# Kernel optimization log

Hardware: AMD Instinct MI355X
Metric: run time of the kernel (lower is better)

Reference implementation:

```python
import jax, jax.numpy as jnp
import numpy as np

N = 50000      # nodes
E = 800000     # edges in adj1/adj2 (avg degree 16)
ED = 400000    # edges after edge-drop
IN = 256       # input feature dim
H = 128        # hidden
H2 = 256       # 2*hidden
GATE = 64


def _xavier(key, shape):
    fan_in, fan_out = shape[0], shape[1]
    lim = np.sqrt(6.0 / (fan_in + fan_out)).astype(np.float32)
    return jax.random.uniform(key, shape, jnp.float32, -lim, lim)


def setup_inputs() -> dict:
    key = jax.random.key(0)
    ks = jax.random.split(key, 20)
    d = {}
    d["x1"] = jax.random.normal(ks[0], (N, IN), jnp.float32)
    d["x2"] = jax.random.normal(ks[1], (N, IN), jnp.float32)
    d["adj1_row"] = jax.random.randint(ks[2], (E,), 0, N, jnp.int32)
    d["adj1_col"] = jax.random.randint(ks[3], (E,), 0, N, jnp.int32)
    d["adj1_val"] = jax.random.uniform(ks[4], (E,), jnp.float32)
    d["adj2_row"] = jax.random.randint(ks[5], (E,), 0, N, jnp.int32)
    d["adj2_col"] = jax.random.randint(ks[6], (E,), 0, N, jnp.int32)
    d["adj2_val"] = jax.random.uniform(ks[7], (E,), jnp.float32)
    d["drop_row"] = jax.random.randint(ks[8], (ED,), 0, N, jnp.int32)
    d["drop_col"] = jax.random.randint(ks[9], (ED,), 0, N, jnp.int32)
    d["drop_val"] = jax.random.uniform(ks[10], (ED,), jnp.float32)
    d["deg"] = jax.random.uniform(ks[11], (N, 1), jnp.float32)
    # GCN layer 0: Linear(IN -> 2H) no bias in fc, plus GCN bias + PReLU
    d["W0"] = _xavier(ks[12], (IN, H2))
    d["b0"] = jnp.zeros((H2,), jnp.float32)
    d["a0"] = jnp.full((1,), 0.25, jnp.float32)  # PReLU param
    # GCN layer 1: Linear(2H -> H)
    d["W1"] = _xavier(ks[13], (H2, H))
    d["b1"] = jnp.zeros((H,), jnp.float32)
    d["a1"] = jnp.full((1,), 0.25, jnp.float32)
    # MLP gate
    d["G1w"] = _xavier(ks[14], (H, GATE))
    d["G1b"] = jnp.zeros((GATE,), jnp.float32)
    d["G2w"] = _xavier(ks[15], (H, GATE))
    d["G2b"] = jnp.zeros((GATE,), jnp.float32)
    d["G3w"] = _xavier(ks[16], (2 * GATE + 1, 1))
    d["G3b"] = jnp.zeros((1,), jnp.float32)
    return d


def _spmm(row, col, val, x, n):
    # sparse adj @ x : gather source features, scale by edge value, scatter-add to rows
    return jax.ops.segment_sum(val[:, None] * x[col], row, num_segments=n)


def _prelu(x, a):
    return jnp.where(x >= 0, x, a * x)


def reference(x1, x2, adj1_row, adj1_col, adj1_val, adj2_row, adj2_col, adj2_val,
              drop_row, drop_col, drop_val, deg,
              W0, b0, a0, W1, b1, a1, G1w, G1b, G2w, G2b, G3w, G3b):
    n = x1.shape[0]

    def gcn(x, row, col, val, W, b, a):
        return _prelu(_spmm(row, col, val, x @ W, n) + b, a)

    def branch(x, row, col, val):
        h = jax.nn.relu(gcn(x, row, col, val, W0, b0, a0))
        return gcn(h, row, col, val, W1, b1, a1)

    # dropout on x1/x2 is identity in eval mode
    h1 = branch(x1, adj1_row, adj1_col, adj1_val)
    h2 = branch(x2, adj1_row, adj1_col, adj1_val)
    h3 = branch(x1, adj2_row, adj2_col, adj2_val)
    h4 = branch(x1, drop_row, drop_col, drop_val)

    # MLP gate on detached h1, h3, deg
    z1 = jax.lax.stop_gradient(h1) @ G1w + G1b
    z2 = jax.lax.stop_gradient(h3) @ G2w + G2b
    w = jnp.concatenate([z1, z2, jax.lax.stop_gradient(deg)], axis=1)
    beta = jax.nn.sigmoid(w @ G3w + G3b)
    return (h1, h2, h3, h4, beta)
```

## Files before the change

### kernel.cpp

```cpp
#include <hip/hip_runtime.h>
#include <hip/hip_bf16.h>

#define H2C 256
#define HDC 128
#define GATEC 64
#define FBSH 9
#define NBF 320
#define EPB 8192
#define EPBH 2048
#define CAPB 10240

typedef unsigned short ushort_t;
typedef unsigned long long ull_t;
typedef __attribute__((ext_vector_type(8))) __bf16 bf16x8;
typedef __attribute__((ext_vector_type(4))) float f32x4;

__device__ inline float bf2f(unsigned short v) {
    union { unsigned u; float f; } t; t.u = ((unsigned)v) << 16; return t.f;
}
__device__ inline unsigned short f2bf(float v) {
    __hip_bfloat16 b = __float2bfloat16(v);
    return *reinterpret_cast<unsigned short*>(&b);
}

__device__ inline void gload_lds16(const void* g, void* l) {
    __builtin_amdgcn_global_load_lds(
        (const __attribute__((address_space(1))) unsigned int*)g,
        (__attribute__((address_space(3))) unsigned int*)l, 16, 0, 0);
}

__global__ __launch_bounds__(256)
void gemm_bf16_mfma(const ushort_t* __restrict__ A, const ushort_t* __restrict__ BT,
                    ushort_t* __restrict__ C, int M, int Nn, int K)
{
    __shared__ ushort_t Alds[128 * 64];
    __shared__ ushort_t Blds[128 * 64];
    const int tid  = threadIdx.x;
    const int w    = tid >> 6;
    const int lane = tid & 63;
    const int wr   = w >> 1;
    const int wc   = w & 1;
    const int bm   = blockIdx.y * 128;
    const int bn   = blockIdx.x * 128;

    f32x4 acc[4][4] = {};

    for (int k0 = 0; k0 < K; k0 += 64) {
        #pragma unroll
        for (int i = 0; i < 4; ++i) {
            const int lin = i * 256 + tid;
            const int r = lin >> 3, p = lin & 7;
            int rm = bm + r; if (rm >= M) rm = M - 1;
            const ushort_t* ga = A + (size_t)rm * K + k0 + ((p ^ (r & 7)) << 3);
            gload_lds16(ga, &Alds[i * 2048 + w * 512]);
        }
        #pragma unroll
        for (int i = 0; i < 4; ++i) {
            const int lin = i * 256 + tid;
            const int r = lin >> 3, p = lin & 7;
            const ushort_t* gb = BT + (size_t)(bn + r) * K + k0 + ((p ^ (r & 7)) << 3);
            gload_lds16(gb, &Blds[i * 2048 + w * 512]);
        }
        __syncthreads();
        #pragma unroll
        for (int kk = 0; kk < 2; ++kk) {
            bf16x8 af[4], bfr[4];
            #pragma unroll
            for (int m = 0; m < 4; ++m) {
                const int r = wr * 64 + m * 16 + (lane & 15);
                const int s = kk * 4 + (lane >> 4);
                af[m] = *reinterpret_cast<const bf16x8*>(&Alds[r * 64 + ((s ^ (r & 7)) << 3)]);
            }
            #pragma unroll
            for (int n = 0; n < 4; ++n) {
                const int r = wc * 64 + n * 16 + (lane & 15);
                const int s = kk * 4 + (lane >> 4);
                bfr[n] = *reinterpret_cast<const bf16x8*>(&Blds[r * 64 + ((s ^ (r & 7)) << 3)]);
            }
            #pragma unroll
            for (int m = 0; m < 4; ++m)
                #pragma unroll
                for (int n = 0; n < 4; ++n)
                    acc[m][n] = __builtin_amdgcn_mfma_f32_16x16x32_bf16(
                        af[m], bfr[n], acc[m][n], 0, 0, 0);
        }
        __syncthreads();
    }

    #pragma unroll
    for (int m = 0; m < 4; ++m) {
        const int row0 = bm + wr * 64 + m * 16 + ((lane >> 4) << 2);
        #pragma unroll
        for (int n = 0; n < 4; ++n) {
            const int col = bn + wc * 64 + n * 16 + (lane & 15);
            #pragma unroll
            for (int q = 0; q < 4; ++q) {
                const int row = row0 + q;
                if (row < M) C[(size_t)row * Nn + col] = f2bf(acc[m][n][q]);
            }
        }
    }
}

__global__ __launch_bounds__(256)
void gemm_xw_f32(const float* __restrict__ X1, const float* __restrict__ X2,
                 const ushort_t* __restrict__ BT, ushort_t* __restrict__ C,
                 int M, int Nn, int K, int Mh)
{
    __shared__ float    Af[128 * 64];
    __shared__ ushort_t Blds[128 * 64];
    const int tid  = threadIdx.x;
    const int w    = tid >> 6;
    const int lane = tid & 63;
    const int wr   = w >> 1;
    const int wc   = w & 1;
    const int bm   = blockIdx.y * 128;
    const int bn   = blockIdx.x * 128;

    f32x4 acc[4][4] = {};

    for (int k0 = 0; k0 < K; k0 += 64) {
        #pragma unroll
        for (int i = 0; i < 8; ++i) {
            const int lin = i * 256 + tid;
            const int r = lin >> 4, q = lin & 15;
            int rm = bm + r; if (rm >= M) rm = M - 1;
            const float* src = ((rm < Mh) ? X1 + (size_t)rm * K
                                          : X2 + (size_t)(rm - Mh) * K)
                               + k0 + ((q ^ (r & 15)) << 2);
            gload_lds16(src, &Af[i * 1024 + w * 256]);
        }
        #pragma unroll
        for (int i = 0; i < 4; ++i) {
            const int lin = i * 256 + tid;
            const int r = lin >> 3, p = lin & 7;
            const ushort_t* gb = BT + (size_t)(bn + r) * K + k0 + ((p ^ (r & 7)) << 3);
            gload_lds16(gb, &Blds[i * 2048 + w * 512]);
        }
        __syncthreads();
        #pragma unroll
        for (int kk = 0; kk < 2; ++kk) {
            bf16x8 af[4], bfr[4];
            #pragma unroll
            for (int m = 0; m < 4; ++m) {
                const int r = wr * 64 + m * 16 + (lane & 15);
                const int s = kk * 4 + (lane >> 4);
                const int rx = r & 15;
                const float4 fa = *reinterpret_cast<const float4*>(
                    &Af[r * 64 + (((2 * s) ^ rx) << 2)]);
                const float4 fb = *reinterpret_cast<const float4*>(
                    &Af[r * 64 + (((2 * s + 1) ^ rx) << 2)]);
                ushort_t t[8] = {f2bf(fa.x), f2bf(fa.y), f2bf(fa.z), f2bf(fa.w),
                                 f2bf(fb.x), f2bf(fb.y), f2bf(fb.z), f2bf(fb.w)};
                af[m] = *reinterpret_cast<bf16x8*>(t);
            }
            #pragma unroll
            for (int n = 0; n < 4; ++n) {
                const int r = wc * 64 + n * 16 + (lane & 15);
                const int s = kk * 4 + (lane >> 4);
                bfr[n] = *reinterpret_cast<const bf16x8*>(&Blds[r * 64 + ((s ^ (r & 7)) << 3)]);
            }
            #pragma unroll
            for (int m = 0; m < 4; ++m)
                #pragma unroll
                for (int n = 0; n < 4; ++n)
                    acc[m][n] = __builtin_amdgcn_mfma_f32_16x16x32_bf16(
                        af[m], bfr[n], acc[m][n], 0, 0, 0);
        }
        __syncthreads();
    }

    #pragma unroll
    for (int m = 0; m < 4; ++m) {
        const int row0 = bm + wr * 64 + m * 16 + ((lane >> 4) << 2);
        #pragma unroll
        for (int n = 0; n < 4; ++n) {
            const int col = bn + wc * 64 + n * 16 + (lane & 15);
            #pragma unroll
            for (int q = 0; q < 4; ++q) {
                const int row = row0 + q;
                if (row < M) C[(size_t)row * Nn + col] = f2bf(acc[m][n][q]);
            }
        }
    }
}

__global__ __launch_bounds__(256)
void transpose2_f2bf_kernel(const float* __restrict__ W0, const float* __restrict__ W1,
                            ushort_t* __restrict__ W0T, ushort_t* __restrict__ W1T)
{
    int i = blockIdx.x * blockDim.x + threadIdx.x;
    if (i < H2C * H2C) {
        const int c = i / H2C, r = i % H2C;
        W0T[(size_t)c * H2C + r] = f2bf(W0[(size_t)r * H2C + c]);
    } else {
        i -= H2C * H2C;
        if (i < H2C * HDC) {
            const int c = i / H2C, r = i % H2C;
            W1T[(size_t)c * H2C + r] = f2bf(W1[(size_t)r * HDC + c]);
        }
    }
}

__global__ __launch_bounds__(256)
void bucket_hist_kernel(const int* __restrict__ r0, const int* __restrict__ r1_,
                        const int* __restrict__ rD, int E, int ED, int N,
                        int* __restrict__ bcnt)
{
    __shared__ int h[NBF];
    const int tid = threadIdx.x;
    for (int t = tid; t < NBF; t += 256) h[t] = 0;
    __syncthreads();
    const long long tot = 2LL * E + ED;
    const long long base = (long long)blockIdx.x * EPBH;
    #pragma unroll
    for (int k = 0; k < EPBH / 256; ++k) {
        const long long i = base + k * 256 + tid;
        if (i < tot) {
            int vr;
            if (i < E)            vr = r0[i];
            else if (i < 2LL * E) vr = N + r1_[i - E];
            else                  vr = 2 * N + rD[i - 2LL * E];
            atomicAdd(&h[vr >> FBSH], 1);
        }
    }
    __syncthreads();
    for (int t = tid; t < NBF; t += 256)
        if (h[t]) atomicAdd(&bcnt[t], h[t]);
}

__global__ void scan_buckets_kernel(const int* __restrict__ bcnt, int nbu, int tot,
                                    int* __restrict__ boff, int* __restrict__ gcur,
                                    int* __restrict__ g, int NR)
{
    if (threadIdx.x == 0) {
        int acc = 0;
        for (int t = 0; t < nbu; ++t) { boff[t] = acc; gcur[t] = acc; acc += bcnt[t]; }
        boff[nbu] = acc;
        g[NR] = tot;
    }
}

__global__ __launch_bounds__(256)
void bucket_stage_kernel(const int* __restrict__ r0, const int* __restrict__ c0, const float* __restrict__ v0,
                         const int* __restrict__ r1, const int* __restrict__ c1, const float* __restrict__ v1,
                         const int* __restrict__ rD, const int* __restrict__ cD, const float* __restrict__ vD,
                         int E, int ED, int N,
                         int* __restrict__ gcur, ull_t* __restrict__ stg)
{
    __shared__ int hcnt[NBF];
    __shared__ int hbase[NBF];
    const int tid = threadIdx.x;
    for (int t = tid; t < NBF; t += 256) hcnt[t] = 0;
    __syncthreads();
    const long long tot = 2LL * E + ED;
    const long long base = (long long)blockIdx.x * EPB;
    #pragma unroll
    for (int k = 0; k < EPB / 256; ++k) {
        const long long i = base + k * 256 + tid;
        if (i < tot) {
            int vr;
            if (i < E)            vr = r0[i];
            else if (i < 2LL * E) vr = N + r1[i - E];
            else                  vr = 2 * N + rD[i - 2LL * E];
            atomicAdd(&hcnt[vr >> FBSH], 1);
        }
    }
    __syncthreads();
    for (int t = tid; t < NBF; t += 256) {
        const int c = hcnt[t];
        hbase[t] = c ? atomicAdd(&gcur[t], c) : 0;
        hcnt[t] = 0;
    }
    __syncthreads();
    #pragma unroll
    for (int k = 0; k < EPB / 256; ++k) {
        const long long i = base + k * 256 + tid;
        if (i < tot) {
            int vr, cc; float vv;
            if (i < E)            { vr = r0[i];                 cc = c0[i];            vv = v0[i]; }
            else if (i < 2LL * E) { vr = N + r1[i - E];         cc = c1[i - E];        vv = v1[i - E]; }
            else                  { vr = 2 * N + rD[i - 2LL * E]; cc = cD[i - 2LL * E]; vv = vD[i - 2LL * E]; }
            const int fb = vr >> FBSH;
            const int p = hbase[fb] + atomicAdd(&hcnt[fb], 1);
            stg[p] = ((ull_t)(unsigned)vr << 32) | ((unsigned)cc << 16) | f2bf(vv);
        }
    }
}

__global__ __launch_bounds__(256)
void sort_bucket_kernel(const int* __restrict__ boff, int NR,
                        const ull_t* __restrict__ stg,
                        int* __restrict__ g, unsigned* __restrict__ ecv)
{
    __shared__ int hcnt[512];
    __shared__ int hscan[512];
    __shared__ unsigned pay[CAPB];
    const int b = blockIdx.x;
    const int r0 = b << FBSH;
    if (r0 >= NR) return;
    int r1 = r0 + (1 << FBSH); if (r1 > NR) r1 = NR;
    const int nrows = r1 - r0;
    const int base = boff[b], end = boff[b + 1];
    const int bsz = end - base;
    const int tid = threadIdx.x;
    hcnt[tid] = 0; hcnt[tid + 256] = 0;
    __syncthreads();
    for (int i = base + tid; i < end; i += 256)
        atomicAdd(&hcnt[(int)(stg[i] >> 32) - r0], 1);
    __syncthreads();
    hscan[tid] = hcnt[tid]; hscan[tid + 256] = hcnt[tid + 256];
    __syncthreads();
    for (int o = 1; o < 512; o <<= 1) {
        const int a0 = (tid >= o) ? hscan[tid - o] : 0;
        const int a1 = (tid + 256 >= o) ? hscan[tid + 256 - o] : 0;
        __syncthreads();
        hscan[tid] += a0; hscan[tid + 256] += a1;
        __syncthreads();
    }
    if (tid < nrows)       g[r0 + tid]       = base + hscan[tid] - hcnt[tid];
    if (tid + 256 < nrows) g[r0 + tid + 256] = base + hscan[tid + 256] - hcnt[tid + 256];
    hcnt[tid]       = hscan[tid] - hcnt[tid];
    hcnt[tid + 256] = hscan[tid + 256] - hcnt[tid + 256];
    __syncthreads();
    if (bsz <= CAPB) {
        for (int i = base + tid; i < end; i += 256) {
            const ull_t t = stg[i];
            const int p = atomicAdd(&hcnt[(int)(t >> 32) - r0], 1);
            pay[p] = (unsigned)t;
        }
        __syncthreads();
        for (int i = tid; i < bsz; i += 256)
            ecv[base + i] = pay[i];
    } else {
        for (int i = base + tid; i < end; i += 256) {
            const ull_t t = stg[i];
            const int p = atomicAdd(&hcnt[(int)(t >> 32) - r0], 1);
            ecv[base + p] = (unsigned)t;
        }
    }
}

__global__ __launch_bounds__(256)
void spmm_f256(const int* __restrict__ rp, const unsigned* __restrict__ ecv,
               const ushort_t* __restrict__ X, ushort_t* __restrict__ Y,
               const float* __restrict__ bias, const float* __restrict__ ap, int n)
{
    const int r = blockIdx.x * 4 + (threadIdx.x >> 6);
    if (r >= n) return;
    const int lane = threadIdx.x & 63;
    const int half = lane >> 5;
    const int l    = lane & 31;
    const int s = rp[r], e = rp[r + 1];
    float acc[8] = {};
    #pragma unroll 4
    for (int j = s + half; j < e; j += 2) {
        const unsigned ev = ecv[j];
        const float v = bf2f((ushort_t)ev);
        const uint4 x = *reinterpret_cast<const uint4*>(X + (size_t)(ev >> 16) * H2C + l * 8);
        acc[0] += v * bf2f((ushort_t)x.x); acc[1] += v * bf2f((ushort_t)(x.x >> 16));
        acc[2] += v * bf2f((ushort_t)x.y); acc[3] += v * bf2f((ushort_t)(x.y >> 16));
        acc[4] += v * bf2f((ushort_t)x.z); acc[5] += v * bf2f((ushort_t)(x.z >> 16));
        acc[6] += v * bf2f((ushort_t)x.w); acc[7] += v * bf2f((ushort_t)(x.w >> 16));
    }
    #pragma unroll
    for (int k = 0; k < 8; ++k) acc[k] += __shfl_xor(acc[k], 32);
    if (half == 0) {
        const float a = ap[0];
        const int f0 = l * 8;
        const float4 b0v = *reinterpret_cast<const float4*>(bias + f0);
        const float4 b1v = *reinterpret_cast<const float4*>(bias + f0 + 4);
        const float bb[8] = {b0v.x, b0v.y, b0v.z, b0v.w, b1v.x, b1v.y, b1v.z, b1v.w};
        unsigned o[4];
        #pragma unroll
        for (int k = 0; k < 8; k += 2) {
            float tx = acc[k] + bb[k];
            float ty = acc[k + 1] + bb[k + 1];
            tx = tx >= 0.f ? tx : a * tx;  ty = ty >= 0.f ? ty : a * ty;
            tx = fmaxf(tx, 0.f);           ty = fmaxf(ty, 0.f);
            o[k >> 1] = ((unsigned)f2bf(ty) << 16) | f2bf(tx);
        }
        *reinterpret_cast<uint4*>(Y + (size_t)r * H2C + f0) = make_uint4(o[0], o[1], o[2], o[3]);
    }
}

__global__ __launch_bounds__(256)
void spmm_f128(const int* __restrict__ rp, const unsigned* __restrict__ ecv,
               const ushort_t* __restrict__ X, float* __restrict__ Y,
               const float* __restrict__ bias, const float* __restrict__ ap, int n)
{
    const int r = blockIdx.x * 4 + (threadIdx.x >> 6);
    if (r >= n) return;
    const int lane = threadIdx.x & 63;
    const int q = lane >> 4;
    const int l = lane & 15;
    const int s = rp[r], e = rp[r + 1];
    float acc[8] = {};
    #pragma unroll 4
    for (int j = s + q; j < e; j += 4) {
        const unsigned ev = ecv[j];
        const float v = bf2f((ushort_t)ev);
        const uint4 x = *reinterpret_cast<const uint4*>(X + (size_t)(ev >> 16) * HDC + l * 8);
        acc[0] += v * bf2f((ushort_t)x.x); acc[1] += v * bf2f((ushort_t)(x.x >> 16));
        acc[2] += v * bf2f((ushort_t)x.y); acc[3] += v * bf2f((ushort_t)(x.y >> 16));
        acc[4] += v * bf2f((ushort_t)x.z); acc[5] += v * bf2f((ushort_t)(x.z >> 16));
        acc[6] += v * bf2f((ushort_t)x.w); acc[7] += v * bf2f((ushort_t)(x.w >> 16));
    }
    #pragma unroll
    for (int k = 0; k < 8; ++k) {
        acc[k] += __shfl_xor(acc[k], 16);
        acc[k] += __shfl_xor(acc[k], 32);
    }
    if (q == 0) {
        const float a = ap[0];
        const int f0 = l * 8;
        const float4 b0v = *reinterpret_cast<const float4*>(bias + f0);
        const float4 b1v = *reinterpret_cast<const float4*>(bias + f0 + 4);
        const float bb[8] = {b0v.x, b0v.y, b0v.z, b0v.w, b1v.x, b1v.y, b1v.z, b1v.w};
        float o[8];
        #pragma unroll
        for (int k = 0; k < 8; ++k) {
            float t = acc[k] + bb[k];
            o[k] = t >= 0.f ? t : a * t;
        }
        *reinterpret_cast<float4*>(Y + (size_t)r * HDC + f0)     = make_float4(o[0], o[1], o[2], o[3]);
        *reinterpret_cast<float4*>(Y + (size_t)r * HDC + f0 + 4) = make_float4(o[4], o[5], o[6], o[7]);
    }
}

__global__ void gate_pre_kernel(const float* __restrict__ G1w, const float* __restrict__ G1b,
                                const float* __restrict__ G2w, const float* __restrict__ G2b,
                                const float* __restrict__ G3w, const float* __restrict__ G3b,
                                float* __restrict__ U)
{
    const int h = threadIdx.x;
    float s1 = 0.f, s2 = 0.f;
    for (int g = 0; g < GATEC; ++g) {
        s1 += G1w[h * GATEC + g] * G3w[g];
        s2 += G2w[h * GATEC + g] * G3w[GATEC + g];
    }
    U[h] = s1;
    U[HDC + h] = s2;
    if (h == 0) {
        float c = G3b[0];
        for (int g = 0; g < GATEC; ++g)
            c += G1b[g] * G3w[g] + G2b[g] * G3w[GATEC + g];
        U[2 * HDC] = c;
        U[2 * HDC + 1] = G3w[2 * GATEC];
    }
}

__global__ __launch_bounds__(256)
void beta_kernel(const float* __restrict__ h1, const float* __restrict__ h3,
                 const float* __restrict__ deg, const float* __restrict__ U,
                 float* __restrict__ beta, int n)
{
    const int i = blockIdx.x * blockDim.x + threadIdx.x;
    if (i >= n) return;
    const float c = U[2 * HDC], wd = U[2 * HDC + 1];
    float s = c + wd * deg[i];
    const float4* h1p = reinterpret_cast<const float4*>(h1 + (size_t)i * HDC);
    const float4* h3p = reinterpret_cast<const float4*>(h3 + (size_t)i * HDC);
    const float4* u1p = reinterpret_cast<const float4*>(U);
    const float4* u2p = reinterpret_cast<const float4*>(U + HDC);
    #pragma unroll 8
    for (int j = 0; j < HDC / 4; ++j) {
        const float4 a = h1p[j], b = u1p[j];
        s += a.x * b.x + a.y * b.y + a.z * b.z + a.w * b.w;
        const float4 a2 = h3p[j], b2 = u2p[j];
        s += a2.x * b2.x + a2.y * b2.y + a2.z * b2.z + a2.w * b2.w;
    }
    beta[i] = 1.f / (1.f + expf(-s));
}

extern "C" void kernel_launch(void* const* d_in, const int* in_sizes, int n_in,
                              void* d_out, int out_size, void* d_ws, size_t ws_size,
                              hipStream_t stream)
{
    const float* x1  = (const float*)d_in[0];
    const float* x2  = (const float*)d_in[1];
    const int*   a1r = (const int*)d_in[2];
    const int*   a1c = (const int*)d_in[3];
    const float* a1v = (const float*)d_in[4];
    const int*   a2r = (const int*)d_in[5];
    const int*   a2c = (const int*)d_in[6];
    const float* a2v = (const float*)d_in[7];
    const int*   dr  = (const int*)d_in[8];
    const int*   dc  = (const int*)d_in[9];
    const float* dv  = (const float*)d_in[10];
    const float* deg = (const float*)d_in[11];
    const float* W0  = (const float*)d_in[12];
    const float* b0  = (const float*)d_in[13];
    const float* a0  = (const float*)d_in[14];
    const float* W1  = (const float*)d_in[15];
    const float* b1  = (const float*)d_in[16];
    const float* a1p = (const float*)d_in[17];
    const float* G1w = (const float*)d_in[18];
    const float* G1b = (const float*)d_in[19];
    const float* G2w = (const float*)d_in[20];
    const float* G2b = (const float*)d_in[21];
    const float* G3w = (const float*)d_in[22];
    const float* G3b = (const float*)d_in[23];

    const int E  = in_sizes[2];
    const int ED = in_sizes[8];
    const int N  = in_sizes[11];
    const int IN = in_sizes[0] / N;
    const long long TOT = 2LL * E + ED;
    const int NR  = 3 * N;
    const int NBUSED = (NR + (1 << FBSH) - 1) >> FBSH;

    char* base = (char*)d_ws;
    size_t off = 0;
    auto alloc = [&](size_t bytes) -> char* {
        char* p = base + off;
        off += (bytes + 255) & ~(size_t)255;
        return p;
    };
    ushort_t* XW12b = (ushort_t*)alloc((size_t)2 * N * H2C * 2);
    char* R = alloc((size_t)N * H2C * 2 + (size_t)N * HDC * 2);
    ull_t*    stg  = (ull_t*)R;
    ushort_t* Bbb  = (ushort_t*)R;
    ushort_t* Cbb  = (ushort_t*)(R + (size_t)N * H2C * 2);
    ushort_t* W0T  = (ushort_t*)alloc((size_t)H2C * H2C * 2);
    ushort_t* W1T  = (ushort_t*)alloc((size_t)HDC * H2C * 2);
    float*    U    = (float*)alloc(258 * 4);
    int*  g       = (int*)alloc((size_t)(NR + 1) * 4);
    int*  bcnt    = (int*)alloc(NBF * 4);
    int*  boff    = (int*)alloc((NBF + 1) * 4);
    int*  gcur    = (int*)alloc(NBF * 4);
    unsigned* ecv = (unsigned*)alloc((size_t)TOT * 4);

    float* out  = (float*)d_out;
    float* h1   = out;
    float* h2   = out + 1 * (size_t)N * HDC;
    float* h3   = out + 2 * (size_t)N * HDC;
    float* h4   = out + 3 * (size_t)N * HDC;
    float* beta = out + 4 * (size_t)N * HDC;

    gate_pre_kernel<<<1, HDC, 0, stream>>>(G1w, G1b, G2w, G2b, G3w, G3b, U);
    transpose2_f2bf_kernel<<<dim3((H2C * H2C + H2C * HDC + 255) / 256), 256, 0, stream>>>(
        W0, W1, W0T, W1T);

    hipMemsetAsync(bcnt, 0, NBF * 4, stream);
    bucket_hist_kernel<<<dim3((unsigned)((TOT + EPBH - 1) / EPBH)), 256, 0, stream>>>(
        a1r, a2r, dr, E, ED, N, bcnt);
    scan_buckets_kernel<<<1, 64, 0, stream>>>(bcnt, NBUSED, (int)TOT, boff, gcur, g, NR);

    bucket_stage_kernel<<<dim3((unsigned)((TOT + EPB - 1) / EPB)), 256, 0, stream>>>(
        a1r, a1c, a1v, a2r, a2c, a2v, dr, dc, dv, E, ED, N, gcur, stg);
    sort_bucket_kernel<<<dim3(NBUSED), 256, 0, stream>>>(boff, NR, stg, g, ecv);

    const int* rp1 = g;
    const int* rp2 = g + N;
    const int* rpD = g + 2 * N;

    gemm_xw_f32<<<dim3(H2C / 128, (2 * N + 127) / 128), 256, 0, stream>>>(
        x1, x2, W0T, XW12b, 2 * N, H2C, IN, N);

    auto run_branch = [&](const int* rp, const ushort_t* Xsrc, float* hout) {
        spmm_f256<<<dim3((N + 3) / 4), 256, 0, stream>>>(rp, ecv, Xsrc, Bbb, b0, a0, N);
        gemm_bf16_mfma<<<dim3(HDC / 128, (N + 127) / 128), 256, 0, stream>>>(
            Bbb, W1T, Cbb, N, HDC, H2C);
        spmm_f128<<<dim3((N + 3) / 4), 256, 0, stream>>>(rp, ecv, Cbb, hout, b1, a1p, N);
    };

    const ushort_t* XW1b = XW12b;
    const ushort_t* XW2b = XW12b + (size_t)N * H2C;

    run_branch(rp1, XW1b, h1);
    run_branch(rp2, XW1b, h3);
    run_branch(rpD, XW1b, h4);
    run_branch(rp1, XW2b, h2);

    beta_kernel<<<dim3((N + 255) / 256), 256, 0, stream>>>(h1, h3, deg, U, beta, N);
}
```

Before: 533.0 us.

## Batch three x1 branches into single SpMM/GEMM launches and halve GEMM K-tile

The three branches that share XW1 (adj1, adj2, drop) now run as one combined SpMM over all 3N concatenated rows, one GEMM, and a new spmm_f128b that routes each row to its output slice. The x2 branch still runs separately. This removes launch overhead and tail effects from nine smaller kernels and gives each launch more parallel work, but it needs larger workspace buffers and a dedicated staging buffer, with a fallback to the old path when the workspace is too small. Separately, the first-layer GEMM K-tile goes from 64 to 32, halving LDS use per block, which may raise occupancy at the cost of more loop iterations and barriers.

```diff
diff --git a/kernel.cpp b/kernel.cpp
--- a/kernel.cpp
+++ b/kernel.cpp
@@ -107,8 +107,8 @@
                  const ushort_t* __restrict__ BT, ushort_t* __restrict__ C,
                  int M, int Nn, int K, int Mh)
 {
-    __shared__ float    Af[128 * 64];
-    __shared__ ushort_t Blds[128 * 64];
+    __shared__ float    Af[128 * 32];
+    __shared__ ushort_t Blds[128 * 32];
     const int tid  = threadIdx.x;
     const int w    = tid >> 6;
     const int lane = tid & 63;
@@ -119,37 +119,36 @@
 
     f32x4 acc[4][4] = {};
 
-    for (int k0 = 0; k0 < K; k0 += 64) {
-        #pragma unroll
-        for (int i = 0; i < 8; ++i) {
+    for (int k0 = 0; k0 < K; k0 += 32) {
+        #pragma unroll
+        for (int i = 0; i < 4; ++i) {
             const int lin = i * 256 + tid;
-            const int r = lin >> 4, q = lin & 15;
+            const int r = lin >> 3, q = lin & 7;
             int rm = bm + r; if (rm >= M) rm = M - 1;
             const float* src = ((rm < Mh) ? X1 + (size_t)rm * K
                                           : X2 + (size_t)(rm - Mh) * K)
-                               + k0 + ((q ^ (r & 15)) << 2);
+                               + k0 + ((q ^ (r & 7)) << 2);
             gload_lds16(src, &Af[i * 1024 + w * 256]);
         }
         #pragma unroll
-        for (int i = 0; i < 4; ++i) {
+        for (int i = 0; i < 2; ++i) {
             const int lin = i * 256 + tid;
-            const int r = lin >> 3, p = lin & 7;
-            const ushort_t* gb = BT + (size_t)(bn + r) * K + k0 + ((p ^ (r & 7)) << 3);
+            const int r = lin >> 2, q = lin & 3;
+            const ushort_t* gb = BT + (size_t)(bn + r) * K + k0 + ((q ^ (r & 3)) << 3);
             gload_lds16(gb, &Blds[i * 2048 + w * 512]);
         }
         __syncthreads();
-        #pragma unroll
-        for (int kk = 0; kk < 2; ++kk) {
+        {
             bf16x8 af[4], bfr[4];
             #pragma unroll
             for (int m = 0; m < 4; ++m) {
                 const int r = wr * 64 + m * 16 + (lane & 15);
-                const int s = kk * 4 + (lane >> 4);
-                const int rx = r & 15;
+                const int s = lane >> 4;
+                const int rx = r & 7;
                 const float4 fa = *reinterpret_cast<const float4*>(
-                    &Af[r * 64 + (((2 * s) ^ rx) << 2)]);
+                    &Af[r * 32 + (((2 * s) ^ rx) << 2)]);
                 const float4 fb = *reinterpret_cast<const float4*>(
-                    &Af[r * 64 + (((2 * s + 1) ^ rx) << 2)]);
+                    &Af[r * 32 + (((2 * s + 1) ^ rx) << 2)]);
                 ushort_t t[8] = {f2bf(fa.x), f2bf(fa.y), f2bf(fa.z), f2bf(fa.w),
                                  f2bf(fb.x), f2bf(fb.y), f2bf(fb.z), f2bf(fb.w)};
                 af[m] = *reinterpret_cast<bf16x8*>(t);
@@ -157,8 +156,8 @@
             #pragma unroll
             for (int n = 0; n < 4; ++n) {
                 const int r = wc * 64 + n * 16 + (lane & 15);
-                const int s = kk * 4 + (lane >> 4);
-                bfr[n] = *reinterpret_cast<const bf16x8*>(&Blds[r * 64 + ((s ^ (r & 7)) << 3)]);
+                const int s = lane >> 4;
+                bfr[n] = *reinterpret_cast<const bf16x8*>(&Blds[r * 32 + ((s ^ (r & 3)) << 3)]);
             }
             #pragma unroll
             for (int m = 0; m < 4; ++m)
@@ -425,6 +424,54 @@
         }
         *reinterpret_cast<float4*>(Y + (size_t)r * HDC + f0)     = make_float4(o[0], o[1], o[2], o[3]);
         *reinterpret_cast<float4*>(Y + (size_t)r * HDC + f0 + 4) = make_float4(o[4], o[5], o[6], o[7]);
+    }
+}
+
+__global__ __launch_bounds__(256)
+void spmm_f128b(const int* __restrict__ rp, const unsigned* __restrict__ ecv,
+                const ushort_t* __restrict__ X, float* __restrict__ out,
+                const float* __restrict__ bias, const float* __restrict__ ap,
+                int n3, int N)
+{
+    const int r = blockIdx.x * 4 + (threadIdx.x >> 6);
+    if (r >= n3) return;
+    const int reg = (r >= 2 * N) ? 2 : ((r >= N) ? 1 : 0);
+    const ushort_t* Xs = X + (size_t)reg * N * HDC;
+    float* Y = out + (size_t)(reg ? r + N : r) * HDC;
+    const int lane = threadIdx.x & 63;
+    const int q = lane >> 4;
+    const int l = lane & 15;
+    const int s = rp[r], e = rp[r + 1];
+    float acc[8] = {};
+    #pragma unroll 4
+    for (int j = s + q; j < e; j += 4) {
+        const unsigned ev = ecv[j];
+        const float v = bf2f((ushort_t)ev);
+        const uint4 x = *reinterpret_cast<const uint4*>(Xs + (size_t)(ev >> 16) * HDC + l * 8);
+        acc[0] += v * bf2f((ushort_t)x.x); acc[1] += v * bf2f((ushort_t)(x.x >> 16));
+        acc[2] += v * bf2f((ushort_t)x.y); acc[3] += v * bf2f((ushort_t)(x.y >> 16));
+        acc[4] += v * bf2f((ushort_t)x.z); acc[5] += v * bf2f((ushort_t)(x.z >> 16));
+        acc[6] += v * bf2f((ushort_t)x.w); acc[7] += v * bf2f((ushort_t)(x.w >> 16));
+    }
+    #pragma unroll
+    for (int k = 0; k < 8; ++k) {
+        acc[k] += __shfl_xor(acc[k], 16);
+        acc[k] += __shfl_xor(acc[k], 32);
+    }
+    if (q == 0) {
+        const float a = ap[0];
+        const int f0 = l * 8;
+        const float4 b0v = *reinterpret_cast<const float4*>(bias + f0);
+        const float4 b1v = *reinterpret_cast<const float4*>(bias + f0 + 4);
+        const float bb[8] = {b0v.x, b0v.y, b0v.z, b0v.w, b1v.x, b1v.y, b1v.z, b1v.w};
+        float o[8];
+        #pragma unroll
+        for (int k = 0; k < 8; ++k) {
+            float t = acc[k] + bb[k];
+            o[k] = t >= 0.f ? t : a * t;
+        }
+        *reinterpret_cast<float4*>(Y + f0)     = make_float4(o[0], o[1], o[2], o[3]);
+        *reinterpret_cast<float4*>(Y + f0 + 4) = make_float4(o[4], o[5], o[6], o[7]);
     }
 }
 
@@ -510,6 +557,17 @@
     const int NR  = 3 * N;
     const int NBUSED = (NR + (1 << FBSH) - 1) >> FBSH;
 
+    auto pad = [](size_t b) { return (b + 255) & ~(size_t)255; };
+
+    size_t need_b = pad((size_t)2 * N * H2C * 2)
+                  + pad((size_t)3 * N * H2C * 2)
+                  + pad((size_t)3 * N * HDC * 2)
+                  + pad((size_t)H2C * H2C * 2) + pad((size_t)HDC * H2C * 2) + pad(258 * 4)
+                  + pad((size_t)(NR + 1) * 4) + pad(NBF * 4) + pad((NBF + 1) * 4) + pad(NBF * 4)
+                  + pad((size_t)TOT * 4)
+                  + pad((size_t)TOT * 8);
+    const bool batched = (ws_size >= need_b);
+
     char* base = (char*)d_ws;
     size_t off = 0;
     auto alloc = [&](size_t bytes) -> char* {
@@ -518,10 +576,18 @@
         return p;
     };
     ushort_t* XW12b = (ushort_t*)alloc((size_t)2 * N * H2C * 2);
-    char* R = alloc((size_t)N * H2C * 2 + (size_t)N * HDC * 2);
-    ull_t*    stg  = (ull_t*)R;
-    ushort_t* Bbb  = (ushort_t*)R;
-    ushort_t* Cbb  = (ushort_t*)(R + (size_t)N * H2C * 2);
+    ull_t* stg; ushort_t *Bb, *Cb;
+    if (batched) {
+        char* R = alloc((size_t)3 * N * H2C * 2);
+        Bb = (ushort_t*)R;
+        Cb = (ushort_t*)alloc((size_t)3 * N * HDC * 2);
+        stg = (ull_t*)alloc((size_t)TOT * 8);
+    } else {
+        char* R = alloc((size_t)N * H2C * 2 + (size_t)N * HDC * 2);
+        stg = (ull_t*)R;
+        Bb  = (ushort_t*)R;
+        Cb  = (ushort_t*)(R + (size_t)N * H2C * 2);
+    }
     ushort_t* W0T  = (ushort_t*)alloc((size_t)H2C * H2C * 2);
     ushort_t* W1T  = (ushort_t*)alloc((size_t)HDC * H2C * 2);
     float*    U    = (float*)alloc(258 * 4);
@@ -551,27 +617,36 @@
         a1r, a1c, a1v, a2r, a2c, a2v, dr, dc, dv, E, ED, N, gcur, stg);
     sort_bucket_kernel<<<dim3(NBUSED), 256, 0, stream>>>(boff, NR, stg, g, ecv);
 
-    const int* rp1 = g;
-    const int* rp2 = g + N;
-    const int* rpD = g + 2 * N;
-
     gemm_xw_f32<<<dim3(H2C / 128, (2 * N + 127) / 128), 256, 0, stream>>>(
         x1, x2, W0T, XW12b, 2 * N, H2C, IN, N);
 
-    auto run_branch = [&](const int* rp, const ushort_t* Xsrc, float* hout) {
-        spmm_f256<<<dim3((N + 3) / 4), 256, 0, stream>>>(rp, ecv, Xsrc, Bbb, b0, a0, N);
-        gemm_bf16_mfma<<<dim3(HDC / 128, (N + 127) / 128), 256, 0, stream>>>(
-            Bbb, W1T, Cbb, N, HDC, H2C);
-        spmm_f128<<<dim3((N + 3) / 4), 256, 0, stream>>>(rp, ecv, Cbb, hout, b1, a1p, N);
-    };
-
     const ushort_t* XW1b = XW12b;
     const ushort_t* XW2b = XW12b + (size_t)N * H2C;
 
-    run_branch(rp1, XW1b, h1);
-    run_branch(rp2, XW1b, h3);
-    run_branch(rpD, XW1b, h4);
-    run_branch(rp1, XW2b, h2);
+    if (batched) {
+        spmm_f256<<<dim3((NR + 3) / 4), 256, 0, stream>>>(g, ecv, XW1b, Bb, b0, a0, NR);
+        gemm_bf16_mfma<<<dim3(HDC / 128, (NR + 127) / 128), 256, 0, stream>>>(
+            Bb, W1T, Cb, NR, HDC, H2C);
+        spmm_f128b<<<dim3((NR + 3) / 4), 256, 0, stream>>>(g, ecv, Cb, out, b1, a1p, NR, N);
+        spmm_f256<<<dim3((N + 3) / 4), 256, 0, stream>>>(g, ecv, XW2b, Bb, b0, a0, N);
+        gemm_bf16_mfma<<<dim3(HDC / 128, (N + 127) / 128), 256, 0, stream>>>(
+            Bb, W1T, Cb, N, HDC, H2C);
+        spmm_f128<<<dim3((N + 3) / 4), 256, 0, stream>>>(g, ecv, Cb, h2, b1, a1p, N);
+    } else {
+        const int* rp1 = g;
+        const int* rp2 = g + N;
+        const int* rpD = g + 2 * N;
+        auto run_branch = [&](const int* rp, const ushort_t* Xsrc, float* hout) {
+            spmm_f256<<<dim3((N + 3) / 4), 256, 0, stream>>>(rp, ecv, Xsrc, Bb, b0, a0, N);
+            gemm_bf16_mfma<<<dim3(HDC / 128, (N + 127) / 128), 256, 0, stream>>>(
+                Bb, W1T, Cb, N, HDC, H2C);
+            spmm_f128<<<dim3((N + 3) / 4), 256, 0, stream>>>(rp, ecv, Cb, hout, b1, a1p, N);
+        };
+        run_branch(rp1, XW1b, h1);
+        run_branch(rp2, XW1b, h3);
+        run_branch(rpD, XW1b, h4);
+        run_branch(rp1, XW2b, h2);
+    }
 
     beta_kernel<<<dim3((N + 255) / 256), 256, 0, stream>>>(h1, h3, deg, U, beta, N);
 }
```

Result: faster. 511.5 us (-4.0%).
